# Kernel optimization log

Hardware: AMD Instinct MI355X
Metric: run time of the kernel (lower is better)

Reference implementation:

```python
import jax, jax.numpy as jnp
import numpy as np

L, B, T, F, C, H, DFF = 2, 4, 2048, 1024, 200, 8, 128


def setup_inputs() -> dict:
    key = jax.random.key(0)
    ks = jax.random.split(key, 12)
    s = 0.02
    return {
        "x": jax.random.normal(ks[0], (B, T, F), jnp.float32),
        "prototypes": jax.random.normal(ks[1], (C, 1, F), jnp.float32),
        # conv_query / conv_key (1x1 convs == linear), per RAB layer
        "wq": jax.random.normal(ks[2], (L, F, F), jnp.float32) * s,
        "bq": jnp.zeros((L, F), jnp.float32),
        "wk": jax.random.normal(ks[3], (L, F, F), jnp.float32) * s,
        "bk": jnp.zeros((L, F), jnp.float32),
        # nn.MultiheadAttention packed in-proj and out-proj
        "in_w": jax.random.normal(ks[4], (L, 3 * F, F), jnp.float32) * s,
        "in_b": jnp.zeros((L, 3 * F), jnp.float32),
        "out_w": jax.random.normal(ks[5], (L, F, F), jnp.float32) * s,
        "out_b": jnp.zeros((L, F), jnp.float32),
        # FFN
        "l1_w": jax.random.normal(ks[6], (L, DFF, F), jnp.float32) * s,
        "l1_b": jnp.zeros((L, DFF), jnp.float32),
        "l2_w": jax.random.normal(ks[7], (L, F, DFF), jnp.float32) * s,
        "l2_b": jnp.zeros((L, F), jnp.float32),
        # LayerNorms
        "ln1_g": jnp.ones((L, F), jnp.float32),
        "ln1_b": jnp.zeros((L, F), jnp.float32),
        "ln2_g": jnp.ones((L, F), jnp.float32),
        "ln2_b": jnp.zeros((L, F), jnp.float32),
        # feature_embedding: Conv1d(F, F, k=3, pad=1) + ReLU
        "emb_w": jax.random.normal(ks[8], (F, F, 3), jnp.float32) * s,
        "emb_b": jnp.zeros((F,), jnp.float32),
    }


def _ln(x, g, b, eps=1e-5):
    mu = jnp.mean(x, axis=-1, keepdims=True)
    var = jnp.mean((x - mu) ** 2, axis=-1, keepdims=True)
    return (x - mu) * jax.lax.rsqrt(var + eps) * g + b


def _mha(q, k, v, w, b, ow, ob):
    # q,k,v: (B,S,F). Packed in-proj like nn.MultiheadAttention (eval: no dropout).
    f = q.shape[-1]
    dh = f // H
    Q = q @ w[:f].T + b[:f]
    K = k @ w[f:2 * f].T + b[f:2 * f]
    V = v @ w[2 * f:].T + b[2 * f:]
    sp = lambda t: t.reshape(t.shape[0], t.shape[1], H, dh)
    scale = np.float32(1.0 / np.sqrt(dh))
    att = jnp.einsum('bqhd,bkhd->bhqk', sp(Q), sp(K)) * scale
    att = jax.nn.softmax(att, axis=-1)
    o = jnp.einsum('bhqk,bkhd->bqhd', att, sp(V)).reshape(q.shape)
    return o @ ow.T + ob


def reference(x, prototypes, wq, bq, wk, bk, in_w, in_b, out_w, out_b,
              l1_w, l1_b, l2_w, l2_b, ln1_g, ln1_b, ln2_g, ln2_b, emb_w, emb_b):
    Bn, Tn, Fn = x.shape
    # torch: prototypes.view(1, F, -1)  (a reshape, NOT a transpose)
    proto = jnp.broadcast_to(prototypes.reshape(1, Fn, -1), (Bn, Fn, prototypes.shape[0]))
    # concat along time: (B,F,S) with S = T + C, then work in (B,S,F)
    src = jnp.swapaxes(jnp.concatenate([jnp.swapaxes(x, 1, 2), proto], axis=2), 1, 2)
    for l in range(L):
        q = src @ wq[l].T + bq[l]          # conv1x1 == pointwise linear
        k = src @ wk[l].T + bk[l]
        a = _mha(q, k, src, in_w[l], in_b[l], out_w[l], out_b[l])
        src = _ln(src + a, ln1_g[l], ln1_b[l])
        ff = jax.nn.relu(src @ l1_w[l].T + l1_b[l]) @ l2_w[l].T + l2_b[l]
        src = _ln(src + ff, ln2_g[l], ln2_b[l])
    feat = jnp.swapaxes(src[:, :Tn], 1, 2)  # (B,F,T): drop prototype tokens
    y = jax.lax.conv_general_dilated(feat, emb_w, (1,), ((1, 1),),
                                     dimension_numbers=('NCH', 'OIH', 'NCH'))
    return jax.nn.relu(y + emb_b[None, :, None])
```

## Files before the change

kernel.cpp:

```cpp
#include <hip/hip_runtime.h>
#include <hip/hip_bf16.h>


constexpr int BN = 4, TN = 2048, FD = 1024, CP = 200, SN = TN + CP;
constexpr int HN = 8, DH = 128, DF = 128, MR = BN * SN;
constexpr int SF = 3 * FD;
constexpr int NT = (SN + 63) / 64;
constexpr float C2 = 0.12751744f;

typedef __attribute__((ext_vector_type(8))) short short8;
typedef __attribute__((ext_vector_type(4))) float f32x4;

__device__ __forceinline__ ushort f2b(float f) {
  union { float f; uint u; } v{f};
  return (ushort)((v.u + 0x7fffu + ((v.u >> 16) & 1u)) >> 16);
}
__device__ __forceinline__ float b2f(ushort u) {
  union { uint u; float f; } v{(uint)u << 16};
  return v.f;
}
__device__ __forceinline__ uint cvt_pk_bf16(float a, float b) {
  uint r;
  asm("v_cvt_pk_bf16_f32 %0, %1, %2" : "=v"(r) : "v"(a), "v"(b));
  return r;
}
__device__ __forceinline__ float exp2_fast(float x) {
  float r;
  asm("v_exp_f32 %0, %1" : "=v"(r) : "v"(x));
  return r;
}
__device__ __forceinline__ void gld16(const void* g, void* l) {
  __builtin_amdgcn_global_load_lds(
      (const __attribute__((address_space(1))) void*)g,
      (__attribute__((address_space(3))) void*)l, 16, 0, 0);
}

__global__ __launch_bounds__(256) void k_build(const float* __restrict__ x,
                                               const float* __restrict__ proto,
                                               ushort* __restrict__ srcb) {
  const int row = blockIdx.x;
  const int b = row / SN, s = row % SN;
  const int f = threadIdx.x * 4;
  const size_t o = (size_t)row * FD + f;
  float4 v;
  if (s < TN) {
    v = *(const float4*)(x + ((size_t)b * TN + s) * FD + f);
  } else {
    const int c = s - TN;
    v.x = proto[(size_t)(f + 0) * CP + c];
    v.y = proto[(size_t)(f + 1) * CP + c];
    v.z = proto[(size_t)(f + 2) * CP + c];
    v.w = proto[(size_t)(f + 3) * CP + c];
  }
  ushort4 u{f2b(v.x), f2b(v.y), f2b(v.z), f2b(v.w)};
  *(ushort4*)(srcb + o) = u;
}

__global__ __launch_bounds__(256) void k_cvt(const float* __restrict__ in,
                                             ushort* __restrict__ out, int n) {
  const int n4 = n >> 2;
  for (int i = blockIdx.x * 256 + threadIdx.x; i < n4; i += gridDim.x * 256) {
    const float4 v = *(const float4*)(in + (size_t)i * 4);
    ushort4 u{f2b(v.x), f2b(v.y), f2b(v.z), f2b(v.w)};
    *(ushort4*)(out + (size_t)i * 4) = u;
  }
}

__global__ __launch_bounds__(256) void k_cvt_inw(const float* __restrict__ in,
                                                 ushort* __restrict__ wInQK,
                                                 ushort* __restrict__ wQKV) {
  constexpr size_t FF = (size_t)FD * FD;
  const int n4 = (int)(6 * FF / 4);
  for (int i = blockIdx.x * 256 + threadIdx.x; i < n4; i += gridDim.x * 256) {
    const size_t idx = (size_t)i * 4;
    const float4 v = *(const float4*)(in + idx);
    ushort4 u{f2b(v.x), f2b(v.y), f2b(v.z), f2b(v.w)};
    const int l = (int)(idx / (3 * FF));
    const size_t r = idx % (3 * FF);
    ushort* dst = (r >= 2 * FF) ? (wQKV + l * 3 * FF + r)
                                : (wInQK + l * 2 * FF + r);
    *(ushort4*)dst = u;
  }
}

__global__ __launch_bounds__(256) void k_cvtT(const float* __restrict__ wq,
                                              const float* __restrict__ wk,
                                              ushort* __restrict__ wT) {
  const int z = blockIdx.z;
  const int qk = z >> 1, l = z & 1;
  const float* W = (qk ? wk : wq) + (size_t)l * FD * FD;
  ushort* WT = wT + (size_t)z * FD * FD;
  __shared__ float t[32][33];
  const int tx = threadIdx.x & 31, ty = threadIdx.x >> 5;
  const int x0 = blockIdx.x * 32, y0 = blockIdx.y * 32;
#pragma unroll
  for (int dy = 0; dy < 4; ++dy)
    t[ty + dy * 8][tx] = W[(size_t)(y0 + ty + dy * 8) * FD + x0 + tx];
  __syncthreads();
#pragma unroll
  for (int dy = 0; dy < 4; ++dy)
    WT[(size_t)(x0 + ty + dy * 8) * FD + y0 + tx] = f2b(t[tx][ty + dy * 8]);
}

__global__ __launch_bounds__(256) void k_vT(const ushort* __restrict__ V,
                                            ushort* __restrict__ Vt) {
  __shared__ ushort t[32][34];
  const int tx = threadIdx.x & 31, ty = threadIdx.x >> 5;
  const int s0 = blockIdx.x * 32, d0 = blockIdx.y * 32, bh = blockIdx.z;
  const int b = bh >> 3, h = bh & 7;
#pragma unroll
  for (int dy = 0; dy < 4; ++dy) {
    const int s = min(s0 + ty + dy * 8, SN - 1);
    t[ty + dy * 8][tx] = V[((size_t)b * SN + s) * SF + h * DH + d0 + tx];
  }
  __syncthreads();
#pragma unroll
  for (int dy = 0; dy < 4; ++dy) {
    const int s = s0 + tx;
    if (s < SN)
      Vt[((size_t)bh * DH + d0 + ty + dy * 8) * SN + s] = t[tx][ty + dy * 8];
  }
}

__global__ __launch_bounds__(256) void k_convw(const float* __restrict__ W,
                                               ushort* __restrict__ out) {
  const int n = FD * FD * 3;
  for (int idx = blockIdx.x * 256 + threadIdx.x; idx < n;
       idx += gridDim.x * 256) {
    const int o = idx / (FD * 3);
    const int rem = idx % (FD * 3);
    const int tau = rem >> 10, i = rem & 1023;
    out[idx] = f2b(W[(size_t)o * (FD * 3) + i * 3 + tau]);
  }
}

__global__ __launch_bounds__(256) void k_pad(const ushort* __restrict__ sb,
                                             ushort* __restrict__ pad) {
  const int r = blockIdx.x, b = blockIdx.y;
  const int f = threadIdx.x * 4;
  ushort4 v{0, 0, 0, 0};
  if (r >= 1 && r <= TN)
    v = *(const ushort4*)(sb + ((size_t)b * SN + (r - 1)) * FD + f);
  *(ushort4*)(pad + ((size_t)b * (TN + 2) + r) * FD + f) = v;
}

__global__ __launch_bounds__(256) void k_beff(const float* __restrict__ in_w,
                                              const float* __restrict__ bvec,
                                              const float* __restrict__ in_b,
                                              float* __restrict__ out, int qk) {
  const int n = blockIdx.x, l = blockIdx.y, tid = threadIdx.x;
  const float* Win = in_w + (size_t)(l * 3 + qk) * FD * FD;
  const float* bv = bvec + (size_t)l * FD;
  float s = 0.f;
  for (int j = tid; j < FD; j += 256) s += Win[(size_t)n * FD + j] * bv[j];
  __shared__ float red[4];
#pragma unroll
  for (int o = 32; o; o >>= 1) s += __shfl_xor(s, o);
  if ((tid & 63) == 0) red[tid >> 6] = s;
  __syncthreads();
  if (tid == 0)
    out[l * 3 * FD + qk * FD + n] =
        red[0] + red[1] + red[2] + red[3] + in_b[l * 3 * FD + qk * FD + n];
}

__global__ __launch_bounds__(256) void k_copyv(const float* __restrict__ in_b,
                                               float* __restrict__ bqkv) {
  const int l = blockIdx.y;
  const int i = blockIdx.x * 256 + threadIdx.x;
  bqkv[l * 3 * FD + 2 * FD + i] = in_b[l * 3 * FD + 2 * FD + i];
}

template <bool RELU, bool BF16OUT, bool PREP4 = false>
__global__ __launch_bounds__(256) void k_mm(const ushort* __restrict__ A,
                                            const ushort* __restrict__ W,
                                            const float* __restrict__ bias,
                                            void* __restrict__ Cv,
                                            int M, int N, int K) {
  constexpr size_t FF = (size_t)FD * FD;
  if (PREP4) {
    const int z = blockIdx.z;
    A += (size_t)z * FF;
    W += (size_t)(((z & 1) * 2) + (z >> 1)) * FF;
    Cv = (void*)((ushort*)Cv + (size_t)((z >> 1) * 3 + (z & 1)) * FF);
  }
  __shared__ __align__(16) ushort As[128 * 32];
  __shared__ __align__(16) ushort Ws[128 * 32];
  const int tid = threadIdx.x;
  const int lane = tid & 63, wv = tid >> 6;
  const int l15 = lane & 15, g = lane >> 4;
  const int wr = wv >> 1, wc = wv & 1;
  int bx = blockIdx.x, by = blockIdx.y;
  const int nwg = gridDim.x * gridDim.y;
  if ((nwg & 7) == 0) {
    int bid = by * gridDim.x + bx;
    bid = (bid & 7) * (nwg >> 3) + (bid >> 3);
    bx = bid % gridDim.x;
    by = bid / gridDim.x;
  }
  const int m0 = by * 128, n0 = bx * 128;
  f32x4 acc[4][4];
#pragma unroll
  for (int i = 0; i < 4; ++i)
#pragma unroll
    for (int j = 0; j < 4; ++j) acc[i][j] = (f32x4){0.f, 0.f, 0.f, 0.f};

  for (int k0 = 0; k0 < K; k0 += 32) {
#pragma unroll
    for (int j = 0; j < 2; ++j) {
      const int u = j * 256 + wv * 64 + lane;
      const int r = u >> 2, c = (u & 3) * 8;
      const int gm = min(m0 + r, M - 1);
      gld16(A + (size_t)gm * K + k0 + c, As + (size_t)u * 8);
    }
#pragma unroll
    for (int j = 0; j < 2; ++j) {
      const int u = j * 256 + wv * 64 + lane;
      const int r = u >> 2, c = (u & 3) * 8;
      gld16(W + (size_t)(n0 + r) * K + k0 + c, Ws + (size_t)u * 8);
    }
    __syncthreads();
    short8 af[4], bfr[4];
#pragma unroll
    for (int i = 0; i < 4; ++i)
      af[i] = *(const short8*)(As + (wr * 64 + i * 16 + l15) * 32 + g * 8);
#pragma unroll
    for (int j = 0; j < 4; ++j)
      bfr[j] = *(const short8*)(Ws + (wc * 64 + j * 16 + l15) * 32 + g * 8);
    __builtin_amdgcn_s_setprio(1);
#pragma unroll
    for (int i = 0; i < 4; ++i)
#pragma unroll
      for (int j = 0; j < 4; ++j)
        acc[i][j] = __builtin_amdgcn_mfma_f32_16x16x32_bf16(af[i], bfr[j],
                                                            acc[i][j], 0, 0, 0);
    __builtin_amdgcn_s_setprio(0);
    __syncthreads();
  }
#pragma unroll
  for (int i = 0; i < 4; ++i) {
#pragma unroll
    for (int r = 0; r < 4; ++r) {
      const int row = m0 + wr * 64 + i * 16 + g * 4 + r;
      if (row >= M) continue;
#pragma unroll
      for (int j = 0; j < 4; ++j) {
        const int col = n0 + wc * 64 + j * 16 + l15;
        float v = acc[i][j][r];
        if (bias) v += bias[col];
        if (RELU) v = fmaxf(v, 0.f);
        if (BF16OUT)
          ((ushort*)Cv)[(size_t)row * N + col] = f2b(v);
        else
          ((float*)Cv)[(size_t)row * N + col] = v;
      }
    }
  }
}

template <bool CONV, bool BF16OUT>
__global__ __launch_bounds__(512, 1) void k_mmB(const ushort* __restrict__ A,
                                                const ushort* __restrict__ W,
                                                const float* __restrict__ bias,
                                                void* __restrict__ Cv,
                                                int M, int N, int K) {
  __shared__ __align__(16) ushort As[2][128 * 64];
  __shared__ __align__(16) ushort Bs[2][256 * 64];
  const int tid = threadIdx.x;
  const int lane = tid & 63, wv = tid >> 6;
  const int l15 = lane & 15, g = lane >> 4;
  const int wr = wv >> 2, wc = wv & 3;
  int bx = blockIdx.x, by = blockIdx.y;
  const int nwg = gridDim.x * gridDim.y;
  if ((nwg & 7) == 0) {
    int bid = by * gridDim.x + bx;
    bid = (bid & 7) * (nwg >> 3) + (bid >> 3);
    bx = bid % gridDim.x;
    by = bid / gridDim.x;
  }
  const int m0 = by * 128, n0 = bx * 256;
  const int NKt = K >> 6;

  f32x4 acc[4][4];
#pragma unroll
  for (int i = 0; i < 4; ++i)
#pragma unroll
    for (int j = 0; j < 4; ++j) acc[i][j] = (f32x4){0.f, 0.f, 0.f, 0.f};

  auto stage = [&](int kt, int d) {
    const int kb = kt * 64;
#pragma unroll
    for (int j = 0; j < 2; ++j) {
      const int u = j * 512 + tid;
      const int row = u >> 3, s = u & 7;
      const int c = s ^ (row & 7);
      const ushort* ga;
      if (CONV) {
        const int rm = m0 + row;
        const int bb = rm >> 11, tt = rm & 2047;
        ga = A + (size_t)(bb * (TN + 2) + tt + (kb >> 10)) * FD + (kb & 1023) +
             c * 8;
      } else {
        ga = A + (size_t)min(m0 + row, M - 1) * K + kb + c * 8;
      }
      gld16(ga, As[d] + row * 64 + s * 8);
    }
#pragma unroll
    for (int j = 0; j < 4; ++j) {
      const int u = j * 512 + tid;
      const int row = u >> 3, s = u & 7;
      const int c = s ^ (row & 7);
      gld16(W + (size_t)(n0 + row) * K + kb + c * 8, Bs[d] + row * 64 + s * 8);
    }
  };

  stage(0, 0);
  for (int kt = 0; kt < NKt; ++kt) {
    const int cur = kt & 1;
    if (kt + 1 < NKt) {
      stage(kt + 1, cur ^ 1);
      asm volatile("s_waitcnt vmcnt(6)" ::: "memory");
    } else {
      asm volatile("s_waitcnt vmcnt(0)" ::: "memory");
    }
    __builtin_amdgcn_s_barrier();
    __builtin_amdgcn_sched_barrier(0);
#pragma unroll
    for (int ks = 0; ks < 2; ++ks) {
      short8 aq[4], bq[4];
#pragma unroll
      for (int mf = 0; mf < 4; ++mf) {
        const int row = wr * 64 + mf * 16 + l15;
        aq[mf] = *(const short8*)(As[cur] + row * 64 +
                                  (((ks * 4 + g) ^ (row & 7)) << 3));
      }
#pragma unroll
      for (int nf = 0; nf < 4; ++nf) {
        const int row = wc * 64 + nf * 16 + l15;
        bq[nf] = *(const short8*)(Bs[cur] + row * 64 +
                                  (((ks * 4 + g) ^ (row & 7)) << 3));
      }
      __builtin_amdgcn_s_setprio(1);
#pragma unroll
      for (int mf = 0; mf < 4; ++mf)
#pragma unroll
        for (int nf = 0; nf < 4; ++nf)
          acc[mf][nf] = __builtin_amdgcn_mfma_f32_16x16x32_bf16(
              aq[mf], bq[nf], acc[mf][nf], 0, 0, 0);
      __builtin_amdgcn_s_setprio(0);
    }
    asm volatile("s_waitcnt lgkmcnt(0)" ::: "memory");
    __builtin_amdgcn_s_barrier();
  }

#pragma unroll
  for (int mf = 0; mf < 4; ++mf) {
#pragma unroll
    for (int r = 0; r < 4; ++r) {
      const int row = m0 + wr * 64 + mf * 16 + g * 4 + r;
      if (!CONV && row >= M) continue;
#pragma unroll
      for (int nf = 0; nf < 4; ++nf) {
        const int col = n0 + wc * 64 + nf * 16 + l15;
        float v = acc[mf][nf][r];
        if (bias) v += bias[col];
        if (CONV) {
          v = fmaxf(v, 0.f);
          const int bb = row >> 11, tt = row & 2047;
          ((float*)Cv)[((size_t)(bb * FD + col)) * TN + tt] = v;
        } else if (BF16OUT) {
          ((ushort*)Cv)[(size_t)row * N + col] = f2b(v);
        } else {
          ((float*)Cv)[(size_t)row * N + col] = v;
        }
      }
    }
  }
}

__global__ __launch_bounds__(512) void k_fattn(const ushort* __restrict__ Qg,
                                               const ushort* __restrict__ Kg,
                                               const ushort* __restrict__ Vt,
                                               ushort* __restrict__ Og) {
  __shared__ __align__(16) ushort Ks[64 * 128];
  __shared__ __align__(16) ushort Vs[128 * 64];
  __shared__ __align__(16) ushort Ps[8][16 * 64];
  const int tid = threadIdx.x, lane = tid & 63, wv = tid >> 6;
  const int l15 = lane & 15, g = lane >> 4;
  const int b = blockIdx.z, h = blockIdx.y, q0 = blockIdx.x * 128;
  const size_t rowBase = (size_t)b * SN;
  const int hoff = h * DH;
  const size_t vbase = (size_t)(b * HN + h) * DH * SN;

  short8 qf[4];
  const int qrow = min(q0 + wv * 16 + l15, SN - 1);
#pragma unroll
  for (int c = 0; c < 4; ++c)
    qf[c] = *(const short8*)(Qg + (rowBase + qrow) * SF + hoff + c * 32 + g * 8);

  short8 onesf;
#pragma unroll
  for (int i = 0; i < 8; ++i) onesf[i] = (short)0x3F80;

  f32x4 o[8];
#pragma unroll
  for (int dt = 0; dt < 8; ++dt) o[dt] = (f32x4){0.f, 0.f, 0.f, 0.f};
  f32x4 lacc = (f32x4){0.f, 0.f, 0.f, 0.f};
  const char* KsB = (const char*)Ks;
  const char* VsB = (const char*)Vs;
  char* PsB = (char*)&Ps[wv][0];

  for (int t = 0; t < NT; ++t) {
    const int kv0 = t * 64;
    const bool tl = (t == NT - 1);
    if (tl) {
#pragma unroll
      for (int j = 0; j < 2; ++j) {
        const int su = j * 512 + tid;
        const int row = su >> 4, s = su & 15;
        const int c16 = s ^ (row & 7);
        const int krow = min(kv0 + row, SN - 1);
        gld16(Kg + (rowBase + krow) * SF + hoff + c16 * 8, Ks + (size_t)su * 8);
      }
#pragma unroll
      for (int j = 0; j < 2; ++j) {
        const int su = j * 512 + tid;
        const int row = su >> 3, s = su & 7;
        const int cc = s ^ (row & 7);
        const int kvc = min(kv0 + cc * 8, SN - 8);
        gld16(Vt + vbase + (size_t)row * SN + kvc, Vs + (size_t)su * 8);
      }
    } else {
#pragma unroll
      for (int j = 0; j < 2; ++j) {
        const int su = j * 512 + tid;
        const int row = su >> 4, s = su & 15;
        const int c16 = s ^ (row & 7);
        gld16(Kg + (rowBase + kv0 + row) * SF + hoff + c16 * 8,
              Ks + (size_t)su * 8);
      }
#pragma unroll
      for (int j = 0; j < 2; ++j) {
        const int su = j * 512 + tid;
        const int row = su >> 3, s = su & 7;
        const int cc = s ^ (row & 7);
        gld16(Vt + vbase + (size_t)row * SN + kv0 + cc * 8,
              Vs + (size_t)su * 8);
      }
    }
    __syncthreads();

    f32x4 st[4];
    __builtin_amdgcn_s_setprio(1);
#pragma unroll
    for (int kt = 0; kt < 4; ++kt) {
      f32x4 s4 = (f32x4){0.f, 0.f, 0.f, 0.f};
      const int row = kt * 16 + l15;
#pragma unroll
      for (int c = 0; c < 4; ++c) {
        const short8 kf = *(const short8*)(
            KsB + row * 256 + (((c * 4 + g) ^ (row & 7)) << 4));
        s4 = __builtin_amdgcn_mfma_f32_16x16x32_bf16(kf, qf[c], s4, 0, 0, 0);
      }
      st[kt] = s4;
    }
    __builtin_amdgcn_s_setprio(0);

    float pfl[16];
    if (tl) {
#pragma unroll
      for (int kt = 0; kt < 4; ++kt)
#pragma unroll
        for (int r = 0; r < 4; ++r) {
          const int kvg = kv0 + kt * 16 + g * 4 + r;
          pfl[kt * 4 + r] = (kvg < SN) ? exp2_fast(C2 * st[kt][r]) : 0.f;
        }
    } else {
#pragma unroll
      for (int i = 0; i < 16; ++i)
        pfl[i] = exp2_fast(C2 * st[i >> 2][i & 3]);
    }

#pragma unroll
    for (int kt = 0; kt < 4; ++kt) {
      const uint lo = cvt_pk_bf16(pfl[kt * 4 + 0], pfl[kt * 4 + 1]);
      const uint hi = cvt_pk_bf16(pfl[kt * 4 + 2], pfl[kt * 4 + 3]);
      const int slot = (kt * 2 + (g >> 1)) ^ (l15 & 7);
      *(uint2*)(PsB + l15 * 128 + slot * 16 + (g & 1) * 8) = make_uint2(lo, hi);
    }

    __builtin_amdgcn_s_setprio(1);
#pragma unroll
    for (int c2 = 0; c2 < 2; ++c2) {
      const int pslot = (c2 * 4 + g) ^ (l15 & 7);
      const short8 pf = *(const short8*)(PsB + l15 * 128 + pslot * 16);
      lacc = __builtin_amdgcn_mfma_f32_16x16x32_bf16(pf, onesf, lacc, 0, 0, 0);
#pragma unroll
      for (int dt = 0; dt < 8; ++dt) {
        const int row = dt * 16 + l15;
        const short8 vf = *(const short8*)(
            VsB + row * 128 + (((c2 * 4 + g) ^ (row & 7)) << 4));
        o[dt] = __builtin_amdgcn_mfma_f32_16x16x32_bf16(pf, vf, o[dt], 0, 0, 0);
      }
    }
    __builtin_amdgcn_s_setprio(0);
    __syncthreads();
  }

  float ir[4];
#pragma unroll
  for (int r = 0; r < 4; ++r) ir[r] = 1.f / lacc[r];
#pragma unroll
  for (int r = 0; r < 4; ++r) {
    const int orow = q0 + wv * 16 + g * 4 + r;
    if (orow >= SN) continue;
#pragma unroll
    for (int dt = 0; dt < 8; ++dt)
      Og[(rowBase + orow) * FD + hoff + dt * 16 + l15] = f2b(o[dt][r] * ir[r]);
  }
}

__global__ __launch_bounds__(256) void k_add_ln(ushort* __restrict__ sb,
                                                const ushort* __restrict__ d,
                                                const float* __restrict__ g,
                                                const float* __restrict__ be) {
  __shared__ float red[4];
  const int row = blockIdx.x;
  const int tid = threadIdx.x;
  const int c = tid * 4;
  const size_t off = (size_t)row * FD + c;
  const ushort4 sv = *(const ushort4*)(sb + off);
  const ushort4 dv = *(const ushort4*)(d + off);
  float v[4] = {b2f(sv.x) + b2f(dv.x), b2f(sv.y) + b2f(dv.y),
                b2f(sv.z) + b2f(dv.z), b2f(sv.w) + b2f(dv.w)};
  float sum = v[0] + v[1] + v[2] + v[3];
#pragma unroll
  for (int o = 32; o; o >>= 1) sum += __shfl_xor(sum, o);
  if ((tid & 63) == 0) red[tid >> 6] = sum;
  __syncthreads();
  sum = red[0] + red[1] + red[2] + red[3];
  const float mu = sum * (1.f / FD);
  float vs = 0.f;
#pragma unroll
  for (int i = 0; i < 4; ++i) {
    const float t = v[i] - mu;
    vs += t * t;
  }
  __syncthreads();
#pragma unroll
  for (int o = 32; o; o >>= 1) vs += __shfl_xor(vs, o);
  if ((tid & 63) == 0) red[tid >> 6] = vs;
  __syncthreads();
  vs = red[0] + red[1] + red[2] + red[3];
  const float rstd = rsqrtf(vs * (1.f / FD) + 1e-5f);
  const float4 gv = *(const float4*)(g + c);
  const float4 bv = *(const float4*)(be + c);
  ushort4 u{f2b((v[0] - mu) * rstd * gv.x + bv.x),
            f2b((v[1] - mu) * rstd * gv.y + bv.y),
            f2b((v[2] - mu) * rstd * gv.z + bv.z),
            f2b((v[3] - mu) * rstd * gv.w + bv.w)};
  *(ushort4*)(sb + off) = u;
}

extern "C" void kernel_launch(void* const* d_in, const int* in_sizes, int n_in,
                              void* d_out, int out_size, void* d_ws,
                              size_t ws_size, hipStream_t stream) {
  const float* x      = (const float*)d_in[0];
  const float* proto  = (const float*)d_in[1];
  const float* wq     = (const float*)d_in[2];
  const float* bq     = (const float*)d_in[3];
  const float* wk     = (const float*)d_in[4];
  const float* bk     = (const float*)d_in[5];
  const float* in_w   = (const float*)d_in[6];
  const float* in_b   = (const float*)d_in[7];
  const float* out_w  = (const float*)d_in[8];
  const float* out_b  = (const float*)d_in[9];
  const float* l1_w   = (const float*)d_in[10];
  const float* l1_b   = (const float*)d_in[11];
  const float* l2_w   = (const float*)d_in[12];
  const float* l2_b   = (const float*)d_in[13];
  const float* ln1_g  = (const float*)d_in[14];
  const float* ln1_b  = (const float*)d_in[15];
  const float* ln2_g  = (const float*)d_in[16];
  const float* ln2_b  = (const float*)d_in[17];
  const float* emb_w  = (const float*)d_in[18];
  const float* emb_b  = (const float*)d_in[19];

  char* p = (char*)d_ws;
  auto take = [&](size_t bytes) {
    char* r = p;
    p += (bytes + 255) & ~(size_t)255;
    return r;
  };
  const size_t MF = (size_t)MR * FD;
  const size_t FF = (size_t)FD * FD;
  ushort* srcb  = (ushort*)take(MF * 2);
  ushort* bQKV  = (ushort*)take((size_t)MR * SF * 2);
  ushort* bVt   = (ushort*)take((size_t)BN * HN * DH * SN * 2);
  ushort* bO    = (ushort*)take(MF * 2);
  ushort* bFF   = (ushort*)take((size_t)MR * DF * 2);
  ushort* wQKV  = (ushort*)take((size_t)2 * 3 * FF * 2);
  ushort* wOut  = (ushort*)take((size_t)2 * FF * 2);
  ushort* wL1   = (ushort*)take((size_t)2 * DF * FD * 2);
  ushort* wL2   = (ushort*)take((size_t)2 * FD * DF * 2);
  float*  bqkv  = (float*)take((size_t)2 * SF * 4);
  ushort* wT     = bQKV;
  ushort* wInQK  = bQKV + 4 * FF;
  ushort* bOut   = bQKV;
  ushort* srcPad = bQKV;
  ushort* convW  = bQKV + (size_t)10 * 1024 * 1024;

  k_build<<<MR, 256, 0, stream>>>(x, proto, srcb);
  k_cvt_inw<<<2048, 256, 0, stream>>>(in_w, wInQK, wQKV);
  k_cvt<<<1024, 256, 0, stream>>>(out_w, wOut, 2 * FF);
  k_cvt<<<256, 256, 0, stream>>>(l1_w, wL1, 2 * DF * FD);
  k_cvt<<<256, 256, 0, stream>>>(l2_w, wL2, 2 * FD * DF);
  k_cvtT<<<dim3(32, 32, 4), 256, 0, stream>>>(wq, wk, wT);
  k_mm<false, true, true><<<dim3(8, 8, 4), 256, 0, stream>>>(
      wInQK, wT, nullptr, wQKV, FD, FD, FD);
  k_beff<<<dim3(FD, 2), 256, 0, stream>>>(in_w, bq, in_b, bqkv, 0);
  k_beff<<<dim3(FD, 2), 256, 0, stream>>>(in_w, bk, in_b, bqkv, 1);
  k_copyv<<<dim3(4, 2), 256, 0, stream>>>(in_b, bqkv);

  const int MB = (MR + 127) / 128;

  for (int l = 0; l < 2; ++l) {
    k_mmB<false, true><<<dim3(SF / 256, MB), 512, 0, stream>>>(
        srcb, wQKV + (size_t)l * 3 * FF, bqkv + (size_t)l * SF, bQKV, MR, SF,
        FD);
    k_vT<<<dim3((SN + 31) / 32, DH / 32, BN * HN), 256, 0, stream>>>(
        bQKV + 2 * FD, bVt);
    k_fattn<<<dim3((SN + 127) / 128, HN, BN), 512, 0, stream>>>(
        bQKV, bQKV + FD, bVt, bO);
    k_mmB<false, true><<<dim3(FD / 256, MB), 512, 0, stream>>>(
        bO, wOut + (size_t)l * FF, out_b + (size_t)l * FD, bOut, MR, FD, FD);
    k_add_ln<<<MR, 256, 0, stream>>>(srcb, bOut, ln1_g + (size_t)l * FD,
                                     ln1_b + (size_t)l * FD);
    k_mm<true, true><<<dim3(DF / 128, MB), 256, 0, stream>>>(
        srcb, wL1 + (size_t)l * DF * FD, l1_b + (size_t)l * DF, bFF, MR, DF,
        FD);
    k_mm<false, true><<<dim3(FD / 128, MB), 256, 0, stream>>>(
        bFF, wL2 + (size_t)l * FD * DF, l2_b + (size_t)l * FD, bOut, MR, FD,
        DF);
    k_add_ln<<<MR, 256, 0, stream>>>(srcb, bOut, ln2_g + (size_t)l * FD,
                                     ln2_b + (size_t)l * FD);
  }

  k_convw<<<1024, 256, 0, stream>>>(emb_w, convW);
  k_pad<<<dim3(TN + 2, BN), 256, 0, stream>>>(srcb, srcPad);
  k_mmB<true, false><<<dim3(FD / 256, (BN * TN) / 128), 512, 0, stream>>>(
      srcPad, convW, emb_b, (float*)d_out, BN * TN, FD, 3 * FD);
}
```

Baseline: 0.9997 ms.

## Double-buffer K/V tiles in flash attention and merge bias kernels

The attention kernel now keeps two LDS buffers for K and V. It issues the global-to-LDS loads for the next tile before computing on the current one, and uses explicit vmcnt waits and raw barriers in place of __syncthreads. This is meant to hide global load latency behind the MFMA work. Separately, the two k_beff launches and the k_copyv launch are merged into one 3D launch to cut launch overhead. The cost is doubled K/V LDS use, which may lower occupancy, and the hand-counted waitcnt values are fragile.

```diff
diff --git a/kernel.cpp b/kernel.cpp
--- a/kernel.cpp
+++ b/kernel.cpp
@@ -145,12 +145,19 @@
 }
 
 __global__ __launch_bounds__(256) void k_beff(const float* __restrict__ in_w,
-                                              const float* __restrict__ bvec,
+                                              const float* __restrict__ bq,
+                                              const float* __restrict__ bk,
                                               const float* __restrict__ in_b,
-                                              float* __restrict__ out, int qk) {
-  const int n = blockIdx.x, l = blockIdx.y, tid = threadIdx.x;
+                                              float* __restrict__ out) {
+  const int n = blockIdx.x, l = blockIdx.y, qk = blockIdx.z;
+  const int tid = threadIdx.x;
+  if (qk == 2) {
+    if (tid == 0)
+      out[l * 3 * FD + 2 * FD + n] = in_b[l * 3 * FD + 2 * FD + n];
+    return;
+  }
   const float* Win = in_w + (size_t)(l * 3 + qk) * FD * FD;
-  const float* bv = bvec + (size_t)l * FD;
+  const float* bv = (qk ? bk : bq) + (size_t)l * FD;
   float s = 0.f;
   for (int j = tid; j < FD; j += 256) s += Win[(size_t)n * FD + j] * bv[j];
   __shared__ float red[4];
@@ -161,13 +168,6 @@
   if (tid == 0)
     out[l * 3 * FD + qk * FD + n] =
         red[0] + red[1] + red[2] + red[3] + in_b[l * 3 * FD + qk * FD + n];
-}
-
-__global__ __launch_bounds__(256) void k_copyv(const float* __restrict__ in_b,
-                                               float* __restrict__ bqkv) {
-  const int l = blockIdx.y;
-  const int i = blockIdx.x * 256 + threadIdx.x;
-  bqkv[l * 3 * FD + 2 * FD + i] = in_b[l * 3 * FD + 2 * FD + i];
 }
 
 template <bool RELU, bool BF16OUT, bool PREP4 = false>
@@ -381,8 +381,8 @@
                                                const ushort* __restrict__ Kg,
                                                const ushort* __restrict__ Vt,
                                                ushort* __restrict__ Og) {
-  __shared__ __align__(16) ushort Ks[64 * 128];
-  __shared__ __align__(16) ushort Vs[128 * 64];
+  __shared__ __align__(16) ushort Ks[2][64 * 128];
+  __shared__ __align__(16) ushort Vs[2][128 * 64];
   __shared__ __align__(16) ushort Ps[8][16 * 64];
   const int tid = threadIdx.x, lane = tid & 63, wv = tid >> 6;
   const int l15 = lane & 15, g = lane >> 4;
@@ -396,6 +396,7 @@
 #pragma unroll
   for (int c = 0; c < 4; ++c)
     qf[c] = *(const short8*)(Qg + (rowBase + qrow) * SF + hoff + c * 32 + g * 8);
+  asm volatile("s_waitcnt vmcnt(0)" ::: "memory");
 
   short8 onesf;
 #pragma unroll
@@ -405,49 +406,47 @@
 #pragma unroll
   for (int dt = 0; dt < 8; ++dt) o[dt] = (f32x4){0.f, 0.f, 0.f, 0.f};
   f32x4 lacc = (f32x4){0.f, 0.f, 0.f, 0.f};
-  const char* KsB = (const char*)Ks;
-  const char* VsB = (const char*)Vs;
   char* PsB = (char*)&Ps[wv][0];
+
+  auto stageK = [&](int kv0, ushort* dst, bool tail) {
+#pragma unroll
+    for (int j = 0; j < 2; ++j) {
+      const int su = j * 512 + tid;
+      const int row = su >> 4, s = su & 15;
+      const int c16 = s ^ (row & 7);
+      const int krow = tail ? min(kv0 + row, SN - 1) : kv0 + row;
+      gld16(Kg + (rowBase + krow) * SF + hoff + c16 * 8, dst + (size_t)su * 8);
+    }
+  };
+  auto stageV = [&](int kv0, ushort* dst, bool tail) {
+#pragma unroll
+    for (int j = 0; j < 2; ++j) {
+      const int su = j * 512 + tid;
+      const int row = su >> 3, s = su & 7;
+      const int cc = s ^ (row & 7);
+      const int kvc = tail ? min(kv0 + cc * 8, SN - 8) : kv0 + cc * 8;
+      gld16(Vt + vbase + (size_t)row * SN + kvc, dst + (size_t)su * 8);
+    }
+  };
+
+  stageK(0, Ks[0], false);
+  stageV(0, Vs[0], false);
 
   for (int t = 0; t < NT; ++t) {
     const int kv0 = t * 64;
-    const bool tl = (t == NT - 1);
-    if (tl) {
-#pragma unroll
-      for (int j = 0; j < 2; ++j) {
-        const int su = j * 512 + tid;
-        const int row = su >> 4, s = su & 15;
-        const int c16 = s ^ (row & 7);
-        const int krow = min(kv0 + row, SN - 1);
-        gld16(Kg + (rowBase + krow) * SF + hoff + c16 * 8, Ks + (size_t)su * 8);
-      }
-#pragma unroll
-      for (int j = 0; j < 2; ++j) {
-        const int su = j * 512 + tid;
-        const int row = su >> 3, s = su & 7;
-        const int cc = s ^ (row & 7);
-        const int kvc = min(kv0 + cc * 8, SN - 8);
-        gld16(Vt + vbase + (size_t)row * SN + kvc, Vs + (size_t)su * 8);
-      }
+    const int cur = t & 1;
+    if (t + 1 < NT) {
+      const bool tl2 = (t + 1 == NT - 1);
+      stageK(kv0 + 64, Ks[cur ^ 1], tl2);
+      stageV(kv0 + 64, Vs[cur ^ 1], tl2);
+      asm volatile("s_waitcnt vmcnt(4)" ::: "memory");
     } else {
-#pragma unroll
-      for (int j = 0; j < 2; ++j) {
-        const int su = j * 512 + tid;
-        const int row = su >> 4, s = su & 15;
-        const int c16 = s ^ (row & 7);
-        gld16(Kg + (rowBase + kv0 + row) * SF + hoff + c16 * 8,
-              Ks + (size_t)su * 8);
-      }
-#pragma unroll
-      for (int j = 0; j < 2; ++j) {
-        const int su = j * 512 + tid;
-        const int row = su >> 3, s = su & 7;
-        const int cc = s ^ (row & 7);
-        gld16(Vt + vbase + (size_t)row * SN + kv0 + cc * 8,
-              Vs + (size_t)su * 8);
-      }
-    }
-    __syncthreads();
+      asm volatile("s_waitcnt vmcnt(0)" ::: "memory");
+    }
+    __builtin_amdgcn_s_barrier();
+    __builtin_amdgcn_sched_barrier(0);
+    const char* KsB = (const char*)Ks[cur];
+    const char* VsB = (const char*)Vs[cur];
 
     f32x4 st[4];
     __builtin_amdgcn_s_setprio(1);
@@ -466,7 +465,7 @@
     __builtin_amdgcn_s_setprio(0);
 
     float pfl[16];
-    if (tl) {
+    if (t == NT - 1) {
 #pragma unroll
       for (int kt = 0; kt < 4; ++kt)
 #pragma unroll
@@ -503,7 +502,8 @@
       }
     }
     __builtin_amdgcn_s_setprio(0);
-    __syncthreads();
+    asm volatile("s_waitcnt lgkmcnt(0)" ::: "memory");
+    __builtin_amdgcn_s_barrier();
   }
 
   float ir[4];
@@ -617,9 +617,7 @@
   k_cvtT<<<dim3(32, 32, 4), 256, 0, stream>>>(wq, wk, wT);
   k_mm<false, true, true><<<dim3(8, 8, 4), 256, 0, stream>>>(
       wInQK, wT, nullptr, wQKV, FD, FD, FD);
-  k_beff<<<dim3(FD, 2), 256, 0, stream>>>(in_w, bq, in_b, bqkv, 0);
-  k_beff<<<dim3(FD, 2), 256, 0, stream>>>(in_w, bk, in_b, bqkv, 1);
-  k_copyv<<<dim3(4, 2), 256, 0, stream>>>(in_b, bqkv);
+  k_beff<<<dim3(FD, 2, 3), 256, 0, stream>>>(in_w, bq, bk, in_b, bqkv);
 
   const int MB = (MR + 127) / 128;
 
```

Result: faster. 971.3 us (-2.8%).
